# Performance work log

Measured on AMD Instinct MI355X. Metric: run time of the kernel, lower is better.

Reference implementation:

```python
import jax, jax.numpy as jnp
import numpy as np

ALPHA = 0.2  # leaky-relu negative slope
NEG_INF = -9e15


def setup_inputs() -> dict:
    key = jax.random.key(0)
    ks = jax.random.split(key, 10)
    bz, N, Fin, Fout = 16, 1024, 1024, 1024
    h = jax.random.normal(ks[0], (bz, N, Fin), dtype=jnp.float32)
    h_xReact = jax.random.normal(ks[1], (bz, N, Fout), dtype=jnp.float32)
    h_oReact = jax.random.normal(ks[2], (bz, N, Fout), dtype=jnp.float32)
    utt_xReact_mask = (jax.random.uniform(ks[3], (bz, N, N)) > 0.5).astype(jnp.float32)
    utt_oReact_mask = (jax.random.uniform(ks[4], (bz, N, N)) > 0.5).astype(jnp.float32)
    W = jax.random.normal(ks[5], (Fin, Fout), dtype=jnp.float32) * 0.02
    a_SS = jax.random.normal(ks[6], (2 * Fout, 1), dtype=jnp.float32) * 0.05
    a_DS = jax.random.normal(ks[7], (2 * Fout, 1), dtype=jnp.float32) * 0.05
    csk_W = jax.random.normal(ks[8], (Fout, Fout), dtype=jnp.float32) * 0.02
    csk_b = jnp.zeros((Fout,), dtype=jnp.float32)
    return {"h": h, "h_xReact": h_xReact, "h_oReact": h_oReact,
            "utt_xReact_mask": utt_xReact_mask, "utt_oReact_mask": utt_oReact_mask,
            "W": W, "a_SS": a_SS, "a_DS": a_DS, "csk_W": csk_W, "csk_b": csk_b}


def _scores(Wh, h_react, a, mask):
    # e[b,i,j] = leaky_relu(Wh[b,i].a1 + (Wh[b,j]+h_react[b,j]).a2) * mask[b,i,j]
    F = Wh.shape[-1]
    a1, a2 = a[:F, 0], a[F:, 0]
    s_src = Wh @ a1                      # [bz, N]
    s_dst = (Wh + h_react) @ a2          # [bz, N]
    e = jax.nn.leaky_relu(s_src[:, :, None] + s_dst[:, None, :], negative_slope=ALPHA)
    return e * mask


def reference(h, h_xReact, h_oReact, utt_xReact_mask, utt_oReact_mask,
              W, a_SS, a_DS, csk_W, csk_b):
    Wh = h @ W                                       # [bz, N, F]
    hx = h_xReact @ csk_W.T + csk_b                  # csk_linear
    ho = h_oReact @ csk_W.T + csk_b
    e_SS = _scores(Wh, hx, a_SS, utt_xReact_mask)    # [bz, N, N]
    e_DS = _scores(Wh, ho, a_DS, utt_oReact_mask)
    e = e_SS + e_DS
    # faithful to source bug: adj uses xReact mask twice
    adj = utt_xReact_mask + utt_xReact_mask
    att = jax.nn.softmax(jnp.where(adj > 0, e, NEG_INF), axis=-1)
    # dropout: eval mode (deterministic reference) -> identity
    h_prime = att @ Wh                               # [bz, N, F]
    return jax.nn.elu(h_prime)                       # concat=True
```

## Files before the change

kernel.cpp:

```cpp
#include <hip/hip_runtime.h>
#include <hip/hip_bf16.h>
#include <math.h>

#define BZ 16
#define NN 1024
#define FF 1024
#define ALPHA 0.2f
#define NEG_INF (-9e15f)

typedef __bf16 bf16x8 __attribute__((ext_vector_type(8)));
typedef __bf16 bf16x4 __attribute__((ext_vector_type(4)));
typedef float  f32x4  __attribute__((ext_vector_type(4)));

#define GLOBAL_AS __attribute__((address_space(1)))
#define LDS_AS    __attribute__((address_space(3)))

__device__ inline void load_lds16(const void* g, void* l) {
    __builtin_amdgcn_global_load_lds((const GLOBAL_AS void*)g, (LDS_AS void*)l, 16, 0, 0);
}

__device__ inline void nt_store64(void* p, const void* v) {
    __builtin_nontemporal_store(*(const unsigned long long*)v, (unsigned long long*)p);
}

__device__ inline float waveAllSum(float v) {
    for (int o = 32; o; o >>= 1) v += __shfl_xor(v, o);
    return v;
}
__device__ inline float waveAllMax(float v) {
    for (int o = 32; o; o >>= 1) v = fmaxf(v, __shfl_xor(v, o));
    return v;
}
__device__ inline float waveReduceSum(float v) {
    for (int o = 32; o; o >>= 1) v += __shfl_down(v, o);
    return v;
}
__device__ inline float dot4(f32x4 a, f32x4 b) {
    return a.x * b.x + a.y * b.y + a.z * b.z + a.w * b.w;
}

template<int EPI>
__global__ __launch_bounds__(512, 2) void gemm256(
    const __bf16* __restrict__ A, const __bf16* __restrict__ Bt,
    float* __restrict__ Cf, __bf16* __restrict__ Ct, size_t sB)
{
    __shared__ char lds[131072];

    const int bid = blockIdx.x;
    const int l   = (bid & 7) * 32 + (bid >> 3);
    const int tileM = (l >> 2) * 256;
    const int tileN = (l & 3) * 256;

    const int tid = threadIdx.x, lane = tid & 63, wid = tid >> 6;
    const int wr = wid >> 2, wc = wid & 3;

    const int batch = tileM >> 10;
    const char* Ab  = (const char*)(A + (size_t)tileM * FF);
    const char* Bbp = (const char*)(Bt + (size_t)batch * sB + (size_t)tileN * FF);

    const int o1 = wid * 1024 + lane * 16;
    const int o2 = o1 + 8192;
    const int r1 = o1 >> 7, r2 = o2 >> 7;
    const size_t raoff1 = (size_t)r1 * 2048 + ((o1 & 127) ^ ((r1 & 7) << 4));
    const size_t raoff2 = (size_t)r2 * 2048 + ((o2 & 127) ^ ((r2 & 7) << 4));

#define STAGE(gb, ldsoff, half, kt) do {                                        \
    const char* g_ = (gb) + (size_t)(half) * (128 * 2048) + (size_t)(kt) * 128; \
    load_lds16(g_ + raoff1, lds + (ldsoff) + (half) * 16384 + wid * 1024);      \
    load_lds16(g_ + raoff2, lds + (ldsoff) + (half) * 16384 + 8192 + wid * 1024);\
} while (0)

    const int fr = lane & 15, kq = lane >> 4;
    const int fswz = (fr & 7) << 4;
    const int ck[2] = { (kq * 16) ^ fswz, (64 + kq * 16) ^ fswz };
    const int abase = (wr * 128 + fr) * 128;
    const int bbase = 32768 + (wc * 64 + fr) * 128;

#define RD(off) (*(const bf16x8*)(lds + (off)))
#define RDA(P, m, kh) RD((P) * 65536 + abase + (m) * 2048 + ck[kh])
#define RDB(P, n, kh) RD((P) * 65536 + bbase + (n) * 2048 + ck[kh])
#define MF16(amr, bvr, m0) do {                                              \
    _Pragma("unroll") for (int n = 0; n < 4; ++n)                            \
    _Pragma("unroll") for (int m = 0; m < 4; ++m)                            \
        acc[m0 + m][n] = __builtin_amdgcn_mfma_f32_16x16x32_bf16(            \
            amr[m], bvr[n], acc[m0 + m][n], 0, 0, 0); } while (0)
#define BAR   __builtin_amdgcn_s_barrier()
#define LGKM0 do { asm volatile("s_waitcnt lgkmcnt(0)" ::: "memory");        \
                   __builtin_amdgcn_sched_barrier(0); } while (0)
#define VM4   asm volatile("s_waitcnt vmcnt(4)" ::: "memory")
#define VM0   asm volatile("s_waitcnt vmcnt(0)" ::: "memory")
#define PRIO1 __builtin_amdgcn_s_setprio(1)
#define PRIO0 __builtin_amdgcn_s_setprio(0)

    f32x4 acc[8][4];
    #pragma unroll
    for (int m = 0; m < 8; ++m)
        #pragma unroll
        for (int n = 0; n < 4; ++n) acc[m][n] = (f32x4){0.f, 0.f, 0.f, 0.f};

    bf16x8 a0[4], a47k0[4], a47k1[4], b0[4], b1[4];

    STAGE(Ab,      0, 0, 0);  STAGE(Ab,      0, 1, 0);
    STAGE(Bbp, 32768, 0, 0);  STAGE(Bbp, 32768, 1, 0);
    STAGE(Bbp, 65536 + 32768, 0, 1);
    STAGE(Ab,  65536,         0, 1);
    VM4; BAR;

    const int NT = FF / 64;
    for (int it = 0; it < NT / 2; ++it) {
        const int t   = 2 * it;
        const int kt1 = t + 1;
        const int kt2 = (t + 2 < NT) ? t + 2 : NT - 1;
        const int kt3 = (t + 3 < NT) ? t + 3 : NT - 1;

        #pragma unroll
        for (int m = 0; m < 4; ++m) a0[m] = RDA(0, m, 0);
        #pragma unroll
        for (int n = 0; n < 4; ++n) b0[n] = RDB(0, n, 0);
        STAGE(Ab, 65536, 1, kt1);
        BAR; LGKM0; PRIO1; MF16(a0, b0, 0); PRIO0; BAR;

        #pragma unroll
        for (int m = 0; m < 4; ++m) a0[m] = RDA(0, m, 1);
        #pragma unroll
        for (int n = 0; n < 4; ++n) b1[n] = RDB(0, n, 1);
        STAGE(Bbp, 65536 + 32768, 1, kt1);
        BAR; LGKM0; PRIO1; MF16(a0, b1, 0); PRIO0; BAR;

        #pragma unroll
        for (int m = 0; m < 4; ++m) { a47k0[m] = RDA(0, 4 + m, 0); a47k1[m] = RDA(0, 4 + m, 1); }
        STAGE(Bbp, 32768, 0, kt2);
        BAR; LGKM0; PRIO1; MF16(a47k0, b0, 4); PRIO0; BAR;

        STAGE(Ab, 0, 0, kt2);
        BAR; PRIO1; MF16(a47k1, b1, 4); PRIO0; VM4; BAR;

        #pragma unroll
        for (int m = 0; m < 4; ++m) a0[m] = RDA(1, m, 0);
        #pragma unroll
        for (int n = 0; n < 4; ++n) b0[n] = RDB(1, n, 0);
        STAGE(Ab, 0, 1, kt2);
        BAR; LGKM0; PRIO1; MF16(a0, b0, 0); PRIO0; BAR;

        #pragma unroll
        for (int m = 0; m < 4; ++m) a0[m] = RDA(1, m, 1);
        #pragma unroll
        for (int n = 0; n < 4; ++n) b1[n] = RDB(1, n, 1);
        STAGE(Bbp, 32768, 1, kt2);
        BAR; LGKM0; PRIO1; MF16(a0, b1, 0); PRIO0; BAR;

        #pragma unroll
        for (int m = 0; m < 4; ++m) { a47k0[m] = RDA(1, 4 + m, 0); a47k1[m] = RDA(1, 4 + m, 1); }
        STAGE(Bbp, 65536 + 32768, 0, kt3);
        BAR; LGKM0; PRIO1; MF16(a47k0, b0, 4); PRIO0; BAR;

        STAGE(Ab, 65536, 0, kt3);
        BAR; PRIO1; MF16(a47k1, b1, 4); PRIO0; VM4; BAR;
    }

    if (EPI == 1) {
        #pragma unroll
        for (int fm = 0; fm < 8; ++fm) {
            const int row0 = tileM + wr * 128 + fm * 16 + kq * 4;
            #pragma unroll
            for (int fn = 0; fn < 4; ++fn) {
                const int col = tileN + wc * 64 + fn * 16 + fr;
                #pragma unroll
                for (int r = 0; r < 4; ++r) {
                    float v = acc[fm][fn][r];
                    v = (v > 0.f) ? v : expm1f(v);
                    Cf[(size_t)(row0 + r) * FF + col] = v;
                }
            }
        }
    } else {
        VM0; BAR;
        char* wlds = lds + wid * 16384;
        #pragma unroll
        for (int fm = 0; fm < 8; ++fm)
            #pragma unroll
            for (int fn = 0; fn < 4; ++fn) {
                const int ccol = fn * 16 + fr;
                const int crow = fm * 16 + kq * 4;
                int addr = (ccol * 256 + crow * 2) ^ ((ccol & 7) << 4);
                bf16x4 v = { (__bf16)acc[fm][fn][0], (__bf16)acc[fm][fn][1],
                             (__bf16)acc[fm][fn][2], (__bf16)acc[fm][fn][3] };
                *(bf16x4*)(wlds + addr) = v;
            }
        const int jb = (tileM & 1023) + wr * 128;
        __bf16* Wt = Ct + (size_t)batch * (1024 * 1024);
        #pragma unroll
        for (int pass = 0; pass < 16; ++pass) {
            const int fl  = pass * 4 + (lane >> 4);
            const int jby = (lane & 15) * 16;
            int addr = (fl * 256 + jby) ^ ((fl & 7) << 4);
            bf16x8 v = *(const bf16x8*)(wlds + addr);
            const int fg = tileN + wc * 64 + fl;
            *(bf16x8*)((char*)(Wt + (size_t)fg * 1024 + jb) + jby) = v;
        }
    }
#undef STAGE
#undef RD
#undef RDA
#undef RDB
#undef MF16
}

__global__ __launch_bounds__(256) void prep_all(
    const float* __restrict__ W, const float* __restrict__ aSS,
    const float* __restrict__ aDS, const float* __restrict__ cskW,
    const float* __restrict__ cskb,
    float* __restrict__ wa, float* __restrict__ vSS, float* __restrict__ vDS,
    float* __restrict__ cv, __bf16* __restrict__ WbfT)
{
    __shared__ char smem[64 * 66 * 2];
    const int bid = blockIdx.x;
    const int t = threadIdx.x;

    if (bid < 1024) {
        const int i = bid;
        float4 w  = ((const float4*)(W + (size_t)i * FF))[t];
        float4 s1 = ((const float4*)aSS)[t];
        float4 s2 = ((const float4*)(aSS + FF))[t];
        float4 d1 = ((const float4*)aDS)[t];
        float4 d2 = ((const float4*)(aDS + FF))[t];
        float v0 = w.x * s1.x + w.y * s1.y + w.z * s1.z + w.w * s1.w;
        float v1 = w.x * s2.x + w.y * s2.y + w.z * s2.z + w.w * s2.w;
        float v2 = w.x * d1.x + w.y * d1.y + w.z * d1.z + w.w * d1.w;
        float v3 = w.x * d2.x + w.y * d2.y + w.z * d2.z + w.w * d2.w;
        v0 = waveReduceSum(v0); v1 = waveReduceSum(v1);
        v2 = waveReduceSum(v2); v3 = waveReduceSum(v3);
        float (*red)[4] = (float (*)[4])smem;
        int wid = t >> 6;
        if ((t & 63) == 0) { red[wid][0] = v0; red[wid][1] = v1; red[wid][2] = v2; red[wid][3] = v3; }
        __syncthreads();
        if (t < 4) {
            float s = red[0][t] + red[1][t] + red[2][t] + red[3][t];
            wa[(size_t)t * FF + i] = s;
        }
    } else if (bid < 1040) {
        const int g0 = (bid - 1024) * 64;
        const int gl = t & 63;
        const int fs = t >> 6;
        const int g = g0 + gl;
        float aS = 0.f, aD = 0.f;
        for (int f = fs * 256; f < fs * 256 + 256; ++f) {
            float w = cskW[(size_t)f * FF + g];
            aS += w * aSS[FF + f];
            aD += w * aDS[FF + f];
        }
        float (*rS)[64] = (float (*)[64])smem;
        float (*rD)[64] = (float (*)[64])(smem + 4 * 64 * 4);
        rS[fs][gl] = aS; rD[fs][gl] = aD;
        __syncthreads();
        if (fs == 0) {
            vSS[g] = rS[0][gl] + rS[1][gl] + rS[2][gl] + rS[3][gl];
            vDS[g] = rD[0][gl] + rD[1][gl] + rD[2][gl] + rD[3][gl];
        }
    } else if (bid == 1040) {
        float cS = 0.f, cD = 0.f;
        for (int f = t; f < FF; f += 256) {
            float bb = cskb[f];
            cS += bb * aSS[FF + f];
            cD += bb * aDS[FF + f];
        }
        cS = waveReduceSum(cS);
        cD = waveReduceSum(cD);
        float* rA = (float*)smem;
        float* rB = (float*)smem + 4;
        int wid = t >> 6;
        if ((t & 63) == 0) { rA[wid] = cS; rB[wid] = cD; }
        __syncthreads();
        if (t == 0) {
            cv[0] = rA[0] + rA[1] + rA[2] + rA[3];
            cv[1] = rB[0] + rB[1] + rB[2] + rB[3];
        }
    } else {
        const int idx2 = bid - 1041;
        const int c0 = (idx2 & 15) * 64;
        const int r0 = (idx2 >> 4) * 64;
        __bf16 (*tt)[66] = (__bf16 (*)[66])smem;
        #pragma unroll
        for (int it = 0; it < 16; ++it) {
            int idx = t + it * 256;
            int r = idx >> 6, c = idx & 63;
            tt[r][c] = (__bf16)W[(size_t)(r0 + r) * FF + c0 + c];
        }
        __syncthreads();
        #pragma unroll
        for (int it = 0; it < 4; ++it) {
            int idx = t + it * 256;
            int rr = idx >> 4;
            int cc = (idx & 15) * 4;
            bf16x4 v = { tt[cc][rr], tt[cc + 1][rr], tt[cc + 2][rr], tt[cc + 3][rr] };
            nt_store64(&WbfT[(size_t)(c0 + rr) * FF + r0 + cc], &v);
        }
    }
}

__global__ __launch_bounds__(256) void scores_all(
    const float* __restrict__ h, const float* __restrict__ hx,
    const float* __restrict__ ho, const float* __restrict__ wa,
    const float* __restrict__ vSS, const float* __restrict__ vDS,
    __bf16* __restrict__ h_bf,
    float* __restrict__ sSrcSS, float* __restrict__ pD1,
    float* __restrict__ sSrcDS, float* __restrict__ pD3,
    float* __restrict__ pD4, float* __restrict__ pD5)
{
    const int wid = threadIdx.x >> 6, lane = threadIdx.x & 63;
    const int row = blockIdx.x * 4 + wid;

    {
        const f32x4* hr  = (const f32x4*)(h + (size_t)row * FF);
        const f32x4* w0p = (const f32x4*)wa;
        const f32x4* w1p = (const f32x4*)(wa + FF);
        const f32x4* w2p = (const f32x4*)(wa + 2 * FF);
        const f32x4* w3p = (const f32x4*)(wa + 3 * FF);

        f32x4 hv[4], w0[4], w1[4], w2[4], w3[4];
        #pragma unroll
        for (int q = 0; q < 4; ++q) hv[q] = hr[q * 64 + lane];
        #pragma unroll
        for (int q = 0; q < 4; ++q) {
            const int i = q * 64 + lane;
            w0[q] = w0p[i]; w1[q] = w1p[i]; w2[q] = w2p[i]; w3[q] = w3p[i];
        }

        bf16x4* hbp = (bf16x4*)(h_bf + (size_t)row * FF);
        #pragma unroll
        for (int q = 0; q < 4; ++q) {
            f32x4 v = hv[q];
            bf16x4 hb = { (__bf16)v.x, (__bf16)v.y, (__bf16)v.z, (__bf16)v.w };
            nt_store64(&hbp[q * 64 + lane], &hb);
        }

        float d0 = 0.f, d1 = 0.f, d2 = 0.f, d3 = 0.f;
        #pragma unroll
        for (int q = 0; q < 4; ++q) {
            d0 += dot4(hv[q], w0[q]);
            d1 += dot4(hv[q], w1[q]);
            d2 += dot4(hv[q], w2[q]);
            d3 += dot4(hv[q], w3[q]);
        }
        d0 = waveAllSum(d0); d1 = waveAllSum(d1);
        d2 = waveAllSum(d2); d3 = waveAllSum(d3);
        if (lane == 0) {
            sSrcSS[row] = d0;
            pD1[row]    = d1;
            sSrcDS[row] = d2;
            pD3[row]    = d3;
        }
    }

    __builtin_amdgcn_sched_barrier(0);

    {
        const f32x4* xr  = (const f32x4*)(hx + (size_t)row * FF);
        const f32x4* orr = (const f32x4*)(ho + (size_t)row * FF);
        const f32x4* vsp = (const f32x4*)vSS;
        const f32x4* vdp = (const f32x4*)vDS;

        f32x4 xv[4], ov[4], vs[4], vd[4];
        #pragma unroll
        for (int q = 0; q < 4; ++q) {
            const int i = q * 64 + lane;
            xv[q] = xr[i]; ov[q] = orr[i];
        }
        #pragma unroll
        for (int q = 0; q < 4; ++q) {
            const int i = q * 64 + lane;
            vs[q] = vsp[i]; vd[q] = vdp[i];
        }

        float d4 = 0.f, d5 = 0.f;
        #pragma unroll
        for (int q = 0; q < 4; ++q) {
            d4 += dot4(xv[q], vs[q]);
            d5 += dot4(ov[q], vd[q]);
        }
        d4 = waveAllSum(d4); d5 = waveAllSum(d5);
        if (lane == 0) {
            pD4[row] = d4;
            pD5[row] = d5;
        }
    }
}

__global__ __launch_bounds__(256) void softmax_att(
    const float* __restrict__ mx, const float* __restrict__ mo,
    const float* __restrict__ sSrcSS, const float* __restrict__ sSrcDS,
    const float* __restrict__ pD1, const float* __restrict__ pD3,
    const float* __restrict__ pD4, const float* __restrict__ pD5,
    const float* __restrict__ cv, __bf16* __restrict__ att)
{
    const int wid = threadIdx.x >> 6, lane = threadIdx.x & 63;
    const int row = blockIdx.x * 4 + wid;
    const int base = row & ~(NN - 1);
    const float srcS = sSrcSS[row];
    const float srcD = sSrcDS[row];
    const float cv0 = cv[0], cv1 = cv[1];
    const f32x4* mxr = (const f32x4*)(mx + (size_t)row * NN);
    const f32x4* mor = (const f32x4*)(mo + (size_t)row * NN);
    const f32x4* p1p = (const f32x4*)(pD1 + base);
    const f32x4* p3p = (const f32x4*)(pD3 + base);
    const f32x4* p4p = (const f32x4*)(pD4 + base);
    const f32x4* p5p = (const f32x4*)(pD5 + base);

    float ev[16];
    float m = -INFINITY;
    #pragma unroll
    for (int q = 0; q < 4; ++q) {
        const int idx = q * 64 + lane;
        f32x4 a = mxr[idx], o = mor[idx];
        f32x4 p1 = p1p[idx], p3 = p3p[idx], p4 = p4p[idx], p5 = p5p[idx];
        #pragma unroll
        for (int l = 0; l < 4; ++l) {
            float eS = srcS + p1[l] + p4[l] + cv0;
            float lS = (eS >= 0.f) ? eS : ALPHA * eS;
            float eD = srcD + p3[l] + p5[l] + cv1;
            float lD = (eD >= 0.f) ? eD : ALPHA * eD;
            float val = (a[l] > 0.f) ? (lS * a[l] + lD * o[l]) : NEG_INF;
            ev[q * 4 + l] = val;
            m = fmaxf(m, val);
        }
    }
    m = waveAllMax(m);

    float s = 0.f;
    #pragma unroll
    for (int i = 0; i < 16; ++i) {
        float p = expf(ev[i] - m);
        ev[i] = p;
        s += p;
    }
    s = waveAllSum(s);
    const float inv = 1.f / s;

    bf16x4* ar = (bf16x4*)(att + (size_t)row * NN);
    #pragma unroll
    for (int q = 0; q < 4; ++q) {
        bf16x4 v = { (__bf16)(ev[q * 4 + 0] * inv), (__bf16)(ev[q * 4 + 1] * inv),
                     (__bf16)(ev[q * 4 + 2] * inv), (__bf16)(ev[q * 4 + 3] * inv) };
        nt_store64(&ar[q * 64 + lane], &v);
    }
}

extern "C" void kernel_launch(void* const* d_in, const int* in_sizes, int n_in,
                              void* d_out, int out_size, void* d_ws, size_t ws_size,
                              hipStream_t stream)
{
    const float* h    = (const float*)d_in[0];
    const float* hx   = (const float*)d_in[1];
    const float* ho   = (const float*)d_in[2];
    const float* mx   = (const float*)d_in[3];
    const float* mo   = (const float*)d_in[4];
    const float* W    = (const float*)d_in[5];
    const float* aSS  = (const float*)d_in[6];
    const float* aDS  = (const float*)d_in[7];
    const float* cskW = (const float*)d_in[8];
    const float* cskb = (const float*)d_in[9];
    float* out = (float*)d_out;

    char* ws = (char*)d_ws;
    const size_t MB = 1024 * 1024;
    __bf16* h_bf   = (__bf16*)ws;
    __bf16* WhT_bf = (__bf16*)(ws + 32 * MB);
    __bf16* att_bf = (__bf16*)(ws + 64 * MB);
    __bf16* WbfT   = (__bf16*)(ws + 96 * MB);
    float* wa     = (float*)(ws + 98 * MB);
    float* vSS    = wa + 4 * FF;
    float* vDS    = vSS + FF;
    float* cv     = vDS + FF;
    float* sSrcSS = cv + 64;
    float* sSrcDS = sSrcSS + BZ * NN;
    float* pD1    = sSrcDS + BZ * NN;
    float* pD3    = pD1 + BZ * NN;
    float* pD4    = pD3 + BZ * NN;
    float* pD5    = pD4 + BZ * NN;

    prep_all<<<1297, 256, 0, stream>>>(W, aSS, aDS, cskW, cskb,
                                       wa, vSS, vDS, cv, WbfT);
    scores_all<<<BZ * NN / 4, 256, 0, stream>>>(h, hx, ho, wa, vSS, vDS, h_bf,
                                                sSrcSS, pD1, sSrcDS, pD3,
                                                pD4, pD5);
    gemm256<2><<<256, 512, 0, stream>>>(h_bf, WbfT, nullptr, WhT_bf, 0);
    softmax_att<<<BZ * NN / 4, 256, 0, stream>>>(mx, mo, sSrcSS, sSrcDS,
                                                 pD1, pD3, pD4, pD5, cv, att_bf);
    gemm256<1><<<256, 512, 0, stream>>>(att_bf, WhT_bf, out, nullptr,
                                        (size_t)NN * FF);
}
```

Measured before the change: 194.5 us.

## Shrink GEMM tile to 256x128 with simpler double-buffered K=32 pipeline

Both bf16 GEMMs now use 256x128 output tiles with a K-step of 32, a 64KB LDS double buffer, and a simple two-stage load/compute loop in place of the 256x256 tile with an interleaved multi-phase schedule. Grid size doubles to 512 blocks, and launch bounds request 4 blocks per CU, aiming for more parallelism and occupancy across the 256 CUs. The trade-off is less data reuse per tile (more global/L2 traffic) and a full vmcnt(0) wait plus barrier every step, which exposes load latency.

After: 207.6 us. 1.07x slower.

```diff
diff --git a/kernel.cpp b/kernel.cpp
--- a/kernel.cpp
+++ b/kernel.cpp
@@ -40,128 +40,88 @@
 }
 
 template<int EPI>
-__global__ __launch_bounds__(512, 2) void gemm256(
+__global__ __launch_bounds__(512, 4) void gemm256(
     const __bf16* __restrict__ A, const __bf16* __restrict__ Bt,
     float* __restrict__ Cf, __bf16* __restrict__ Ct, size_t sB)
 {
-    __shared__ char lds[131072];
+    __shared__ char lds[65536];
 
     const int bid = blockIdx.x;
-    const int l   = (bid & 7) * 32 + (bid >> 3);
-    const int tileM = (l >> 2) * 256;
-    const int tileN = (l & 3) * 256;
+    const int l   = (bid & 7) * 64 + (bid >> 3);
+    const int tileM = (l >> 3) * 256;
+    const int tileN = (l & 7) * 128;
 
     const int tid = threadIdx.x, lane = tid & 63, wid = tid >> 6;
-    const int wr = wid >> 2, wc = wid & 3;
+    const int wr = wid >> 1, wc = wid & 1;
 
     const int batch = tileM >> 10;
     const char* Ab  = (const char*)(A + (size_t)tileM * FF);
     const char* Bbp = (const char*)(Bt + (size_t)batch * sB + (size_t)tileN * FF);
 
-    const int o1 = wid * 1024 + lane * 16;
-    const int o2 = o1 + 8192;
-    const int r1 = o1 >> 7, r2 = o2 >> 7;
-    const size_t raoff1 = (size_t)r1 * 2048 + ((o1 & 127) ^ ((r1 & 7) << 4));
-    const size_t raoff2 = (size_t)r2 * 2048 + ((o2 & 127) ^ ((r2 & 7) << 4));
-
-#define STAGE(gb, ldsoff, half, kt) do {                                        \
-    const char* g_ = (gb) + (size_t)(half) * (128 * 2048) + (size_t)(kt) * 128; \
-    load_lds16(g_ + raoff1, lds + (ldsoff) + (half) * 16384 + wid * 1024);      \
-    load_lds16(g_ + raoff2, lds + (ldsoff) + (half) * 16384 + 8192 + wid * 1024);\
+    const int sr = tid >> 2, ss = tid & 3;
+    const size_t srcA0 = (size_t)sr * 2048 + (size_t)((ss ^ ((sr >> 1) & 3)) << 4);
+    const size_t srcA1 = srcA0 + (size_t)128 * 2048;
+    const size_t srcB0 = srcA0;
+
+#define STAGE(buf, kt) do {                                                   \
+    const size_t ko = (size_t)(kt) * 64;                                      \
+    load_lds16(Ab + srcA0 + ko, lds + (buf) * 16384 + tid * 16);              \
+    load_lds16(Ab + srcA1 + ko, lds + (buf) * 16384 + 8192 + tid * 16);       \
+    load_lds16(Bbp + srcB0 + ko, lds + 32768 + (buf) * 8192 + tid * 16);      \
 } while (0)
 
     const int fr = lane & 15, kq = lane >> 4;
-    const int fswz = (fr & 7) << 4;
-    const int ck[2] = { (kq * 16) ^ fswz, (64 + kq * 16) ^ fswz };
-    const int abase = (wr * 128 + fr) * 128;
-    const int bbase = 32768 + (wc * 64 + fr) * 128;
+    const int slotx = (kq ^ ((fr >> 1) & 3)) << 4;
+    const int abase = (wr * 64 + fr) * 64 + slotx;
+    const int bbase = (wc * 64 + fr) * 64 + slotx;
 
 #define RD(off) (*(const bf16x8*)(lds + (off)))
-#define RDA(P, m, kh) RD((P) * 65536 + abase + (m) * 2048 + ck[kh])
-#define RDB(P, n, kh) RD((P) * 65536 + bbase + (n) * 2048 + ck[kh])
-#define MF16(amr, bvr, m0) do {                                              \
-    _Pragma("unroll") for (int n = 0; n < 4; ++n)                            \
-    _Pragma("unroll") for (int m = 0; m < 4; ++m)                            \
-        acc[m0 + m][n] = __builtin_amdgcn_mfma_f32_16x16x32_bf16(            \
-            amr[m], bvr[n], acc[m0 + m][n], 0, 0, 0); } while (0)
+#define RDA(buf, m) RD((buf) * 16384 + abase + (m) * 1024)
+#define RDB(buf, n) RD(32768 + (buf) * 8192 + bbase + (n) * 1024)
 #define BAR   __builtin_amdgcn_s_barrier()
 #define LGKM0 do { asm volatile("s_waitcnt lgkmcnt(0)" ::: "memory");        \
                    __builtin_amdgcn_sched_barrier(0); } while (0)
-#define VM4   asm volatile("s_waitcnt vmcnt(4)" ::: "memory")
 #define VM0   asm volatile("s_waitcnt vmcnt(0)" ::: "memory")
 #define PRIO1 __builtin_amdgcn_s_setprio(1)
 #define PRIO0 __builtin_amdgcn_s_setprio(0)
-
-    f32x4 acc[8][4];
+#define MF16(buf) do {                                                        \
+    _Pragma("unroll") for (int m = 0; m < 4; ++m) a[m] = RDA(buf, m);         \
+    _Pragma("unroll") for (int n = 0; n < 4; ++n) b[n] = RDB(buf, n);         \
+    LGKM0; PRIO1;                                                             \
+    _Pragma("unroll") for (int n = 0; n < 4; ++n)                             \
+    _Pragma("unroll") for (int m = 0; m < 4; ++m)                             \
+        acc[m][n] = __builtin_amdgcn_mfma_f32_16x16x32_bf16(                  \
+            a[m], b[n], acc[m][n], 0, 0, 0);                                  \
+    PRIO0; } while (0)
+
+    f32x4 acc[4][4];
     #pragma unroll
-    for (int m = 0; m < 8; ++m)
+    for (int m = 0; m < 4; ++m)
         #pragma unroll
         for (int n = 0; n < 4; ++n) acc[m][n] = (f32x4){0.f, 0.f, 0.f, 0.f};
 
-    bf16x8 a0[4], a47k0[4], a47k1[4], b0[4], b1[4];
-
-    STAGE(Ab,      0, 0, 0);  STAGE(Ab,      0, 1, 0);
-    STAGE(Bbp, 32768, 0, 0);  STAGE(Bbp, 32768, 1, 0);
-    STAGE(Bbp, 65536 + 32768, 0, 1);
-    STAGE(Ab,  65536,         0, 1);
-    VM4; BAR;
-
-    const int NT = FF / 64;
+    bf16x8 a[4], b[4];
+
+    STAGE(0, 0);
+    VM0; BAR;
+
+    const int NT = FF / 32;
     for (int it = 0; it < NT / 2; ++it) {
-        const int t   = 2 * it;
-        const int kt1 = t + 1;
-        const int kt2 = (t + 2 < NT) ? t + 2 : NT - 1;
-        const int kt3 = (t + 3 < NT) ? t + 3 : NT - 1;
-
-        #pragma unroll
-        for (int m = 0; m < 4; ++m) a0[m] = RDA(0, m, 0);
-        #pragma unroll
-        for (int n = 0; n < 4; ++n) b0[n] = RDB(0, n, 0);
-        STAGE(Ab, 65536, 1, kt1);
-        BAR; LGKM0; PRIO1; MF16(a0, b0, 0); PRIO0; BAR;
-
-        #pragma unroll
-        for (int m = 0; m < 4; ++m) a0[m] = RDA(0, m, 1);
-        #pragma unroll
-        for (int n = 0; n < 4; ++n) b1[n] = RDB(0, n, 1);
-        STAGE(Bbp, 65536 + 32768, 1, kt1);
-        BAR; LGKM0; PRIO1; MF16(a0, b1, 0); PRIO0; BAR;
-
-        #pragma unroll
-        for (int m = 0; m < 4; ++m) { a47k0[m] = RDA(0, 4 + m, 0); a47k1[m] = RDA(0, 4 + m, 1); }
-        STAGE(Bbp, 32768, 0, kt2);
-        BAR; LGKM0; PRIO1; MF16(a47k0, b0, 4); PRIO0; BAR;
-
-        STAGE(Ab, 0, 0, kt2);
-        BAR; PRIO1; MF16(a47k1, b1, 4); PRIO0; VM4; BAR;
-
-        #pragma unroll
-        for (int m = 0; m < 4; ++m) a0[m] = RDA(1, m, 0);
-        #pragma unroll
-        for (int n = 0; n < 4; ++n) b0[n] = RDB(1, n, 0);
-        STAGE(Ab, 0, 1, kt2);
-        BAR; LGKM0; PRIO1; MF16(a0, b0, 0); PRIO0; BAR;
-
-        #pragma unroll
-        for (int m = 0; m < 4; ++m) a0[m] = RDA(1, m, 1);
-        #pragma unroll
-        for (int n = 0; n < 4; ++n) b1[n] = RDB(1, n, 1);
-        STAGE(Bbp, 32768, 1, kt2);
-        BAR; LGKM0; PRIO1; MF16(a0, b1, 0); PRIO0; BAR;
-
-        #pragma unroll
-        for (int m = 0; m < 4; ++m) { a47k0[m] = RDA(1, 4 + m, 0); a47k1[m] = RDA(1, 4 + m, 1); }
-        STAGE(Bbp, 65536 + 32768, 0, kt3);
-        BAR; LGKM0; PRIO1; MF16(a47k0, b0, 4); PRIO0; BAR;
-
-        STAGE(Ab, 65536, 0, kt3);
-        BAR; PRIO1; MF16(a47k1, b1, 4); PRIO0; VM4; BAR;
+        const int t0  = 2 * it;
+        const int kt1 = t0 + 1;
+        const int kt2 = (t0 + 2 < NT) ? t0 + 2 : NT - 1;
+        STAGE(1, kt1);
+        MF16(0);
+        VM0; BAR;
+        STAGE(0, kt2);
+        MF16(1);
+        VM0; BAR;
     }
 
     if (EPI == 1) {
         #pragma unroll
-        for (int fm = 0; fm < 8; ++fm) {
-            const int row0 = tileM + wr * 128 + fm * 16 + kq * 4;
+        for (int fm = 0; fm < 4; ++fm) {
+            const int row0 = tileM + wr * 64 + fm * 16 + kq * 4;
             #pragma unroll
             for (int fn = 0; fn < 4; ++fn) {
                 const int col = tileN + wc * 64 + fn * 16 + fr;
@@ -174,26 +134,26 @@
             }
         }
     } else {
-        VM0; BAR;
-        char* wlds = lds + wid * 16384;
-        #pragma unroll
-        for (int fm = 0; fm < 8; ++fm)
+        char* wlds = lds + wid * 8192;
+        #pragma unroll
+        for (int fm = 0; fm < 4; ++fm)
             #pragma unroll
             for (int fn = 0; fn < 4; ++fn) {
                 const int ccol = fn * 16 + fr;
                 const int crow = fm * 16 + kq * 4;
-                int addr = (ccol * 256 + crow * 2) ^ ((ccol & 7) << 4);
+                int addr = (ccol * 128 + crow * 2) ^ ((ccol & 7) << 4);
                 bf16x4 v = { (__bf16)acc[fm][fn][0], (__bf16)acc[fm][fn][1],
                              (__bf16)acc[fm][fn][2], (__bf16)acc[fm][fn][3] };
                 *(bf16x4*)(wlds + addr) = v;
             }
-        const int jb = (tileM & 1023) + wr * 128;
+        __syncthreads();
+        const int jb = (tileM & 1023) + wr * 64;
         __bf16* Wt = Ct + (size_t)batch * (1024 * 1024);
         #pragma unroll
-        for (int pass = 0; pass < 16; ++pass) {
-            const int fl  = pass * 4 + (lane >> 4);
-            const int jby = (lane & 15) * 16;
-            int addr = (fl * 256 + jby) ^ ((fl & 7) << 4);
+        for (int pass = 0; pass < 8; ++pass) {
+            const int fl  = pass * 8 + (lane >> 3);
+            const int jby = (lane & 7) * 16;
+            int addr = (fl * 128 + jby) ^ ((fl & 7) << 4);
             bf16x8 v = *(const bf16x8*)(wlds + addr);
             const int fg = tileN + wc * 64 + fl;
             *(bf16x8*)((char*)(Wt + (size_t)fg * 1024 + jb) + jby) = v;
@@ -483,9 +443,9 @@
     scores_all<<<BZ * NN / 4, 256, 0, stream>>>(h, hx, ho, wa, vSS, vDS, h_bf,
                                                 sSrcSS, pD1, sSrcDS, pD3,
                                                 pD4, pD5);
-    gemm256<2><<<256, 512, 0, stream>>>(h_bf, WbfT, nullptr, WhT_bf, 0);
+    gemm256<2><<<512, 512, 0, stream>>>(h_bf, WbfT, nullptr, WhT_bf, 0);
     softmax_att<<<BZ * NN / 4, 256, 0, stream>>>(mx, mo, sSrcSS, sSrcDS,
                                                  pD1, pD3, pD4, pD5, cv, att_bf);
-    gemm256<1><<<256, 512, 0, stream>>>(att_bf, WhT_bf, out, nullptr,
+    gemm256<1><<<512, 512, 0, stream>>>(att_bf, WhT_bf, out, nullptr,
                                         (size_t)NN * FF);
 }
```

## Fuse attention score projections into Wh GEMM epilogue via partial sums

Applied to the files above, without the earlier changes.

Instead of precomputing W·a vectors in prep and dotting them with h in scores_all, the Wh GEMM epilogue now dots its bf16-accumulated tile with the a vectors. It reduces across lanes and waves in LDS and writes per-column-tile partial sums, which softmax_att adds together. This removes 1024 prep blocks and the per-row fp32 dot products over h, at the cost of extra epilogue work, two extra barriers, and four times more partial-score reads in softmax. Scores are now computed from bf16-rounded inputs with fp32 accumulation rather than the exact fp32 h·(W a).

Result: slower. 219.7 us (+13.0%).

```diff
diff --git a/kernel.cpp b/kernel.cpp
--- a/kernel.cpp
+++ b/kernel.cpp
@@ -42,7 +42,9 @@
 template<int EPI>
 __global__ __launch_bounds__(512, 2) void gemm256(
     const __bf16* __restrict__ A, const __bf16* __restrict__ Bt,
-    float* __restrict__ Cf, __bf16* __restrict__ Ct, size_t sB)
+    float* __restrict__ Cf, __bf16* __restrict__ Ct, size_t sB,
+    const float* __restrict__ aSS, const float* __restrict__ aDS,
+    float* __restrict__ pA)
 {
     __shared__ char lds[131072];
 
@@ -50,6 +52,7 @@
     const int l   = (bid & 7) * 32 + (bid >> 3);
     const int tileM = (l >> 2) * 256;
     const int tileN = (l & 3) * 256;
+    const int nIdx  = l & 3;
 
     const int tid = threadIdx.x, lane = tid & 63, wid = tid >> 6;
     const int wr = wid >> 2, wc = wid & 3;
@@ -175,6 +178,54 @@
         }
     } else {
         VM0; BAR;
+        {
+            float aq0[4], aq1[4], aq2[4], aq3[4];
+            #pragma unroll
+            for (int fn = 0; fn < 4; ++fn) {
+                const int colF = tileN + wc * 64 + fn * 16 + fr;
+                aq0[fn] = aSS[colF];
+                aq1[fn] = aSS[FF + colF];
+                aq2[fn] = aDS[colF];
+                aq3[fn] = aDS[FF + colF];
+            }
+            float* dred = (float*)lds;
+            #pragma unroll
+            for (int fm = 0; fm < 8; ++fm) {
+                #pragma unroll
+                for (int r = 0; r < 4; ++r) {
+                    float p0 = 0.f, p1 = 0.f, p2 = 0.f, p3 = 0.f;
+                    #pragma unroll
+                    for (int fn = 0; fn < 4; ++fn) {
+                        float v = acc[fm][fn][r];
+                        p0 += v * aq0[fn]; p1 += v * aq1[fn];
+                        p2 += v * aq2[fn]; p3 += v * aq3[fn];
+                    }
+                    for (int o = 1; o < 16; o <<= 1) {
+                        p0 += __shfl_xor(p0, o); p1 += __shfl_xor(p1, o);
+                        p2 += __shfl_xor(p2, o); p3 += __shfl_xor(p3, o);
+                    }
+                    if (fr == 0) {
+                        const int row = wr * 128 + fm * 16 + kq * 4 + r;
+                        float* d = dred + ((size_t)wc * 256 + row) * 4;
+                        d[0] = p0; d[1] = p1; d[2] = p2; d[3] = p3;
+                    }
+                }
+            }
+            BAR;
+            if (tid < 256) {
+                const int row = tid;
+                const size_t M = (size_t)BZ * NN;
+                #pragma unroll
+                for (int q = 0; q < 4; ++q) {
+                    float s = dred[((size_t)0 * 256 + row) * 4 + q]
+                            + dred[((size_t)1 * 256 + row) * 4 + q]
+                            + dred[((size_t)2 * 256 + row) * 4 + q]
+                            + dred[((size_t)3 * 256 + row) * 4 + q];
+                    pA[((size_t)q * 4 + nIdx) * M + tileM + row] = s;
+                }
+            }
+            BAR;
+        }
         char* wlds = lds + wid * 16384;
         #pragma unroll
         for (int fm = 0; fm < 8; ++fm)
@@ -210,36 +261,15 @@
     const float* __restrict__ W, const float* __restrict__ aSS,
     const float* __restrict__ aDS, const float* __restrict__ cskW,
     const float* __restrict__ cskb,
-    float* __restrict__ wa, float* __restrict__ vSS, float* __restrict__ vDS,
+    float* __restrict__ vSS, float* __restrict__ vDS,
     float* __restrict__ cv, __bf16* __restrict__ WbfT)
 {
     __shared__ char smem[64 * 66 * 2];
     const int bid = blockIdx.x;
     const int t = threadIdx.x;
 
-    if (bid < 1024) {
-        const int i = bid;
-        float4 w  = ((const float4*)(W + (size_t)i * FF))[t];
-        float4 s1 = ((const float4*)aSS)[t];
-        float4 s2 = ((const float4*)(aSS + FF))[t];
-        float4 d1 = ((const float4*)aDS)[t];
-        float4 d2 = ((const float4*)(aDS + FF))[t];
-        float v0 = w.x * s1.x + w.y * s1.y + w.z * s1.z + w.w * s1.w;
-        float v1 = w.x * s2.x + w.y * s2.y + w.z * s2.z + w.w * s2.w;
-        float v2 = w.x * d1.x + w.y * d1.y + w.z * d1.z + w.w * d1.w;
-        float v3 = w.x * d2.x + w.y * d2.y + w.z * d2.z + w.w * d2.w;
-        v0 = waveReduceSum(v0); v1 = waveReduceSum(v1);
-        v2 = waveReduceSum(v2); v3 = waveReduceSum(v3);
-        float (*red)[4] = (float (*)[4])smem;
-        int wid = t >> 6;
-        if ((t & 63) == 0) { red[wid][0] = v0; red[wid][1] = v1; red[wid][2] = v2; red[wid][3] = v3; }
-        __syncthreads();
-        if (t < 4) {
-            float s = red[0][t] + red[1][t] + red[2][t] + red[3][t];
-            wa[(size_t)t * FF + i] = s;
-        }
-    } else if (bid < 1040) {
-        const int g0 = (bid - 1024) * 64;
+    if (bid < 16) {
+        const int g0 = bid * 64;
         const int gl = t & 63;
         const int fs = t >> 6;
         const int g = g0 + gl;
@@ -257,7 +287,7 @@
             vSS[g] = rS[0][gl] + rS[1][gl] + rS[2][gl] + rS[3][gl];
             vDS[g] = rD[0][gl] + rD[1][gl] + rD[2][gl] + rD[3][gl];
         }
-    } else if (bid == 1040) {
+    } else if (bid == 16) {
         float cS = 0.f, cD = 0.f;
         for (int f = t; f < FF; f += 256) {
             float bb = cskb[f];
@@ -276,7 +306,7 @@
             cv[1] = rB[0] + rB[1] + rB[2] + rB[3];
         }
     } else {
-        const int idx2 = bid - 1041;
+        const int idx2 = bid - 17;
         const int c0 = (idx2 & 15) * 64;
         const int r0 = (idx2 >> 4) * 64;
         __bf16 (*tt)[66] = (__bf16 (*)[66])smem;
@@ -300,55 +330,25 @@
 
 __global__ __launch_bounds__(256) void scores_all(
     const float* __restrict__ h, const float* __restrict__ hx,
-    const float* __restrict__ ho, const float* __restrict__ wa,
+    const float* __restrict__ ho,
     const float* __restrict__ vSS, const float* __restrict__ vDS,
     __bf16* __restrict__ h_bf,
-    float* __restrict__ sSrcSS, float* __restrict__ pD1,
-    float* __restrict__ sSrcDS, float* __restrict__ pD3,
     float* __restrict__ pD4, float* __restrict__ pD5)
 {
     const int wid = threadIdx.x >> 6, lane = threadIdx.x & 63;
     const int row = blockIdx.x * 4 + wid;
 
     {
-        const f32x4* hr  = (const f32x4*)(h + (size_t)row * FF);
-        const f32x4* w0p = (const f32x4*)wa;
-        const f32x4* w1p = (const f32x4*)(wa + FF);
-        const f32x4* w2p = (const f32x4*)(wa + 2 * FF);
-        const f32x4* w3p = (const f32x4*)(wa + 3 * FF);
-
-        f32x4 hv[4], w0[4], w1[4], w2[4], w3[4];
+        const f32x4* hr = (const f32x4*)(h + (size_t)row * FF);
+        f32x4 hv[4];
         #pragma unroll
         for (int q = 0; q < 4; ++q) hv[q] = hr[q * 64 + lane];
-        #pragma unroll
-        for (int q = 0; q < 4; ++q) {
-            const int i = q * 64 + lane;
-            w0[q] = w0p[i]; w1[q] = w1p[i]; w2[q] = w2p[i]; w3[q] = w3p[i];
-        }
-
         bf16x4* hbp = (bf16x4*)(h_bf + (size_t)row * FF);
         #pragma unroll
         for (int q = 0; q < 4; ++q) {
             f32x4 v = hv[q];
             bf16x4 hb = { (__bf16)v.x, (__bf16)v.y, (__bf16)v.z, (__bf16)v.w };
             nt_store64(&hbp[q * 64 + lane], &hb);
-        }
-
-        float d0 = 0.f, d1 = 0.f, d2 = 0.f, d3 = 0.f;
-        #pragma unroll
-        for (int q = 0; q < 4; ++q) {
-            d0 += dot4(hv[q], w0[q]);
-            d1 += dot4(hv[q], w1[q]);
-            d2 += dot4(hv[q], w2[q]);
-            d3 += dot4(hv[q], w3[q]);
-        }
-        d0 = waveAllSum(d0); d1 = waveAllSum(d1);
-        d2 = waveAllSum(d2); d3 = waveAllSum(d3);
-        if (lane == 0) {
-            sSrcSS[row] = d0;
-            pD1[row]    = d1;
-            sSrcDS[row] = d2;
-            pD3[row]    = d3;
         }
     }
 
@@ -388,21 +388,32 @@
 
 __global__ __launch_bounds__(256) void softmax_att(
     const float* __restrict__ mx, const float* __restrict__ mo,
-    const float* __restrict__ sSrcSS, const float* __restrict__ sSrcDS,
-    const float* __restrict__ pD1, const float* __restrict__ pD3,
+    const float* __restrict__ pA,
     const float* __restrict__ pD4, const float* __restrict__ pD5,
     const float* __restrict__ cv, __bf16* __restrict__ att)
 {
     const int wid = threadIdx.x >> 6, lane = threadIdx.x & 63;
     const int row = blockIdx.x * 4 + wid;
     const int base = row & ~(NN - 1);
-    const float srcS = sSrcSS[row];
-    const float srcD = sSrcDS[row];
+    const size_t M = (size_t)BZ * NN;
+
+    float srcS = 0.f, srcD = 0.f;
+    #pragma unroll
+    for (int n = 0; n < 4; ++n) {
+        srcS += pA[((size_t)0 * 4 + n) * M + row];
+        srcD += pA[((size_t)2 * 4 + n) * M + row];
+    }
     const float cv0 = cv[0], cv1 = cv[1];
     const f32x4* mxr = (const f32x4*)(mx + (size_t)row * NN);
     const f32x4* mor = (const f32x4*)(mo + (size_t)row * NN);
-    const f32x4* p1p = (const f32x4*)(pD1 + base);
-    const f32x4* p3p = (const f32x4*)(pD3 + base);
+    const f32x4* p1n0 = (const f32x4*)(pA + ((size_t)1 * 4 + 0) * M + base);
+    const f32x4* p1n1 = (const f32x4*)(pA + ((size_t)1 * 4 + 1) * M + base);
+    const f32x4* p1n2 = (const f32x4*)(pA + ((size_t)1 * 4 + 2) * M + base);
+    const f32x4* p1n3 = (const f32x4*)(pA + ((size_t)1 * 4 + 3) * M + base);
+    const f32x4* p3n0 = (const f32x4*)(pA + ((size_t)3 * 4 + 0) * M + base);
+    const f32x4* p3n1 = (const f32x4*)(pA + ((size_t)3 * 4 + 1) * M + base);
+    const f32x4* p3n2 = (const f32x4*)(pA + ((size_t)3 * 4 + 2) * M + base);
+    const f32x4* p3n3 = (const f32x4*)(pA + ((size_t)3 * 4 + 3) * M + base);
     const f32x4* p4p = (const f32x4*)(pD4 + base);
     const f32x4* p5p = (const f32x4*)(pD5 + base);
 
@@ -412,7 +423,9 @@
     for (int q = 0; q < 4; ++q) {
         const int idx = q * 64 + lane;
         f32x4 a = mxr[idx], o = mor[idx];
-        f32x4 p1 = p1p[idx], p3 = p3p[idx], p4 = p4p[idx], p5 = p5p[idx];
+        f32x4 p1 = p1n0[idx] + p1n1[idx] + p1n2[idx] + p1n3[idx];
+        f32x4 p3 = p3n0[idx] + p3n1[idx] + p3n2[idx] + p3n3[idx];
+        f32x4 p4 = p4p[idx], p5 = p5p[idx];
         #pragma unroll
         for (int l = 0; l < 4; ++l) {
             float eS = srcS + p1[l] + p4[l] + cv0;
@@ -467,25 +480,21 @@
     __bf16* WhT_bf = (__bf16*)(ws + 32 * MB);
     __bf16* att_bf = (__bf16*)(ws + 64 * MB);
     __bf16* WbfT   = (__bf16*)(ws + 96 * MB);
-    float* wa     = (float*)(ws + 98 * MB);
-    float* vSS    = wa + 4 * FF;
+    float* pA     = (float*)(ws + 98 * MB);
+    float* vSS    = pA + 16 * (size_t)BZ * NN;
     float* vDS    = vSS + FF;
     float* cv     = vDS + FF;
-    float* sSrcSS = cv + 64;
-    float* sSrcDS = sSrcSS + BZ * NN;
-    float* pD1    = sSrcDS + BZ * NN;
-    float* pD3    = pD1 + BZ * NN;
-    float* pD4    = pD3 + BZ * NN;
+    float* pD4    = cv + 64;
     float* pD5    = pD4 + BZ * NN;
 
-    prep_all<<<1297, 256, 0, stream>>>(W, aSS, aDS, cskW, cskb,
-                                       wa, vSS, vDS, cv, WbfT);
-    scores_all<<<BZ * NN / 4, 256, 0, stream>>>(h, hx, ho, wa, vSS, vDS, h_bf,
-                                                sSrcSS, pD1, sSrcDS, pD3,
+    prep_all<<<273, 256, 0, stream>>>(W, aSS, aDS, cskW, cskb,
+                                      vSS, vDS, cv, WbfT);
+    scores_all<<<BZ * NN / 4, 256, 0, stream>>>(h, hx, ho, vSS, vDS, h_bf,
                                                 pD4, pD5);
-    gemm256<2><<<256, 512, 0, stream>>>(h_bf, WbfT, nullptr, WhT_bf, 0);
-    softmax_att<<<BZ * NN / 4, 256, 0, stream>>>(mx, mo, sSrcSS, sSrcDS,
-                                                 pD1, pD3, pD4, pD5, cv, att_bf);
+    gemm256<2><<<256, 512, 0, stream>>>(h_bf, WbfT, nullptr, WhT_bf, 0,
+                                        aSS, aDS, pA);
+    softmax_att<<<BZ * NN / 4, 256, 0, stream>>>(mx, mo, pA, pD4, pD5, cv,
+                                                 att_bf);
     gemm256<1><<<256, 512, 0, stream>>>(att_bf, WhT_bf, out, nullptr,
-                                        (size_t)NN * FF);
-}
+                                        (size_t)NN * FF, aSS, aDS, nullptr);
+}
```
